# Kernel tuning notes

Hardware: AMD Instinct MI355X
Metric: run time of the kernel (lower is better)

Reference implementation:

```python
import jax, jax.numpy as jnp
import numpy as np

B, C, H, W = 8, 256, 128, 128


def _bilinear_sample(img, gx, gy):
    """F.grid_sample(bilinear, padding_mode='zeros', align_corners=False).
    img: [B,C,H,W]; gx, gy: [B,H,W] normalized coords in [-1,1].
    Returns [B,C,H,W]."""
    Bi, Ci, Hi, Wi = img.shape
    ix = ((gx + 1.0) * Wi - 1.0) * 0.5  # pixel x coord
    iy = ((gy + 1.0) * Hi - 1.0) * 0.5  # pixel y coord
    ix0 = jnp.floor(ix)
    iy0 = jnp.floor(iy)
    wx1 = ix - ix0
    wy1 = iy - iy0
    bidx = jnp.arange(Bi)[:, None, None]

    def gather(iyf, ixf):
        valid = (ixf >= 0) & (ixf < Wi) & (iyf >= 0) & (iyf < Hi)
        iyc = jnp.clip(iyf, 0, Hi - 1).astype(jnp.int32)
        ixc = jnp.clip(ixf, 0, Wi - 1).astype(jnp.int32)
        v = img[bidx, :, iyc, ixc]  # [B,H,W,C]
        return jnp.where(valid[..., None], v, jnp.zeros((), img.dtype))

    v00 = gather(iy0, ix0)
    v01 = gather(iy0, ix0 + 1)
    v10 = gather(iy0 + 1, ix0)
    v11 = gather(iy0 + 1, ix0 + 1)
    w00 = ((1.0 - wy1) * (1.0 - wx1))[..., None]
    w01 = ((1.0 - wy1) * wx1)[..., None]
    w10 = (wy1 * (1.0 - wx1))[..., None]
    w11 = (wy1 * wx1)[..., None]
    out = v00 * w00 + v01 * w01 + v10 * w10 + v11 * w11  # [B,H,W,C]
    return out.transpose(0, 3, 1, 2)


def setup_inputs() -> dict:
    key = jax.random.key(0)
    ks = jax.random.split(key, 7)
    s = 1.0 / np.sqrt(C)
    return {
        "x": jax.random.normal(ks[0], (B, C, H, W), jnp.float32),
        "w_dw": jax.random.normal(ks[1], (C,), jnp.float32) * s,        # depthwise 1x1, no bias
        "w_off": jax.random.normal(ks[2], (2, C), jnp.float32) * s,     # offset 1x1 conv C->2
        "b_off": jax.random.normal(ks[3], (2,), jnp.float32) * 0.1,
        "w_pc": jax.random.normal(ks[4], (C, C), jnp.float32) * s,      # pointwise 1x1, no bias
        "w_W": jax.random.normal(ks[5], (C, C), jnp.float32) * s,       # residual-merge 1x1 conv
        "b_W": jax.random.normal(ks[6], (C,), jnp.float32) * 0.1,
    }


def reference(x, w_dw, w_off, b_off, w_pc, w_W, b_W):
    # offset = tanh(Conv1x1(x)) -> one shared (dx, dy) field (group == inplanes)
    offset = jnp.tanh(jnp.einsum('oc,bchw->bohw', w_off, x) + b_off[None, :, None, None])
    # depthwise 1x1 conv (bias=False) == per-channel scale
    dw = x * w_dw[None, :, None, None]
    # base normalized grid: X varies along W, Y along H (np.meshgrid convention)
    gx_base = jnp.linspace(-1.0, 1.0, W)[None, None, :]  # [1,1,W]
    gy_base = jnp.linspace(-1.0, 1.0, H)[None, :, None]  # [1,H,1]
    gx = jnp.clip(gx_base + offset[:, 0], -1.0, 1.0)  # [B,H,W]
    gy = jnp.clip(gy_base + offset[:, 1], -1.0, 1.0)
    sampled = _bilinear_sample(dw, gx, gy)             # [B,C,H,W]
    out = jnp.einsum('oc,bchw->bohw', w_pc, sampled)   # pointwise conv
    out = jnp.einsum('oc,bchw->bohw', w_W, out) + b_W[None, :, None, None]
    return out + x
```

## Files before the change

### kernel.cpp

```cpp
#include <hip/hip_runtime.h>
#include <hip/hip_bf16.h>

#define Bn 8
#define Cn 256
#define Hn 128
#define Wn 128
#define HWn (Hn * Wn)

typedef __attribute__((ext_vector_type(8))) short bfrag8;
typedef __attribute__((ext_vector_type(8))) unsigned short u16x8;
typedef __attribute__((ext_vector_type(4))) float f32x4;
typedef __attribute__((ext_vector_type(4))) unsigned int u32x4;

__device__ __forceinline__ float bf2f(unsigned short u) {
    unsigned int v = ((unsigned int)u) << 16;
    return __builtin_bit_cast(float, v);
}
__device__ __forceinline__ unsigned short f2bf(float f) {
    unsigned int u = __builtin_bit_cast(unsigned int, f);
    unsigned int lsb = (u >> 16) & 1u;
    u += 0x7fffu + lsb;
    return (unsigned short)(u >> 16);
}

__device__ __forceinline__ void load_lds16(const void* g, void* l) {
    __builtin_amdgcn_global_load_lds(
        (const __attribute__((address_space(1))) unsigned int*)g,
        (__attribute__((address_space(3))) unsigned int*)l,
        16, 0, 0);
}

__global__ __launch_bounds__(256)
void build_wcomb(const float* __restrict__ w_dw,
                 const float* __restrict__ w_pc,
                 const float* __restrict__ w_W,
                 unsigned short* __restrict__ wfrag) {
    const int o = blockIdx.x;
    const int c = threadIdx.x;
    float acc = 0.f;
#pragma unroll 8
    for (int k = 0; k < Cn; ++k)
        acc = fmaf(w_W[o * Cn + k], w_pc[k * Cn + c], acc);
    const int ob = o >> 4, lr = o & 15;
    const int ks = c >> 5, lg = (c & 31) >> 3, e = c & 7;
    const int lane = (lg << 4) + lr;
    wfrag[((((ob << 3) + ks) << 6) + lane) * 8 + e] = f2bf(acc * w_dw[c]);
}

__global__ __launch_bounds__(512, 2)
void prep_kernel(const float* __restrict__ x,
                 const float* __restrict__ w_off,
                 const float* __restrict__ b_off,
                 unsigned short* __restrict__ x_t,
                 float2* __restrict__ coords) {
    __shared__ __align__(16) char tile[256 * 256];
    __shared__ float woT[2][256];
    const int t = threadIdx.x;
    const int lane = t & 63;
    const int wv = t >> 6;
    int blk = blockIdx.x;
    blk = ((blk & 7) << 8) | (blk >> 3);
    const int b = blk >> 8;
    const int p0 = (blk & 255) << 6;
    const float* xp = x + ((size_t)b * Cn) * HWn + p0;

    {
        const int s = t >> 8, c = t & 255;
        woT[s][((c & 7) << 5) | (c >> 3)] = w_off[(s << 8) + c];
    }

    {
        const int r = lane >> 4;
        const int q = lane & 15;
#pragma unroll
        for (int i = 0; i < 8; ++i) {
            const int cbase = (wv << 5) + (i << 2);
            const int c = cbase + r;
            const int swz = (c ^ (c >> 4)) & 15;
            const float* src = xp + (size_t)c * HWn + ((q ^ swz) << 2);
            load_lds16(src, tile + (cbase << 8));
        }
    }
    __syncthreads();

    {
        const int m = lane >> 5;
        const int octet = lane & 31;
#pragma unroll
        for (int i = 0; i < 4; ++i) {
            const int px = (wv << 3) + (i << 1) + m;
            float s0 = 0.f, s1 = 0.f;
            u16x8 res;
#pragma unroll
            for (int j = 0; j < 8; ++j) {
                const int c = (octet << 3) + j;
                const int swz = (c ^ (c >> 4)) & 15;
                const int byte = (c << 8) + ((((px >> 2) ^ swz)) << 4) + ((px & 3) << 2);
                float v = *reinterpret_cast<const float*>(tile + byte);
                s0 = fmaf(v, woT[0][(j << 5) + octet], s0);
                s1 = fmaf(v, woT[1][(j << 5) + octet], s1);
                res[j] = f2bf(v);
            }
            *reinterpret_cast<u16x8*>(
                x_t + ((size_t)(b * HWn + p0 + px)) * Cn + (octet << 3)) = res;

            s0 += __shfl_xor(s0, 1); s0 += __shfl_xor(s0, 2); s0 += __shfl_xor(s0, 4);
            s0 += __shfl_xor(s0, 8); s0 += __shfl_xor(s0, 16);
            s1 += __shfl_xor(s1, 1); s1 += __shfl_xor(s1, 2); s1 += __shfl_xor(s1, 4);
            s1 += __shfl_xor(s1, 8); s1 += __shfl_xor(s1, 16);
            if (octet == 0) {
                float o0 = tanhf(s0 + b_off[0]);
                float o1 = tanhf(s1 + b_off[1]);
                int p = p0 + px;
                int yy = p >> 7, xx = p & 127;
                float gx = fminf(fmaxf(-1.f + xx * (2.f / 127.f) + o0, -1.f), 1.f);
                float gy = fminf(fmaxf(-1.f + yy * (2.f / 127.f) + o1, -1.f), 1.f);
                coords[(size_t)b * HWn + p] = make_float2(gx * 64.f + 63.5f, gy * 64.f + 63.5f);
            }
        }
    }
}

__global__ __launch_bounds__(512, 2)
void main_kernel(const float* __restrict__ x,
                 const float* __restrict__ b_W,
                 const unsigned short* __restrict__ x_t,
                 const float2* __restrict__ coords,
                 const unsigned short* __restrict__ wfrag,
                 float* __restrict__ out) {
    __shared__ __align__(16) char As[4][32 * 512];
    __shared__ __align__(16) float4 wts[32];
    const int t = threadIdx.x;
    const int lane = t & 63;
    const int wid = t >> 6;
    int blk = blockIdx.x;
    blk = ((blk & 7) << 9) | (blk >> 3);
    const int b = blk >> 9;
    const int p0 = (blk & 511) << 5;
    const size_t pixbase = (size_t)b * HWn + p0;
    const unsigned short* xtb = x_t + (size_t)b * HWn * Cn;

    if (t < 32) {
        float2 co = coords[pixbase + t];
        float ix = co.x, iy = co.y;
        float fx = floorf(ix), fy = floorf(iy);
        int ix0 = (int)fx, iy0 = (int)fy;
        float wx1 = ix - fx, wy1 = iy - fy;
        float wx0 = 1.f - wx1, wy0 = 1.f - wy1;
        bool vx0 = (ix0 >= 0) && (ix0 < Wn);
        bool vx1 = (ix0 >= -1) && (ix0 < Wn - 1);
        bool vy0 = (iy0 >= 0) && (iy0 < Hn);
        bool vy1 = (iy0 >= -1) && (iy0 < Hn - 1);
        float4 w;
        w.x = (vy0 && vx0) ? wy0 * wx0 : 0.f;
        w.y = (vy0 && vx1) ? wy0 * wx1 : 0.f;
        w.z = (vy1 && vx0) ? wy1 * wx0 : 0.f;
        w.w = (vy1 && vx1) ? wy1 * wx1 : 0.f;
        wts[t] = w;
    }

    {
        const int hp = lane >> 5;
        const int j = lane & 31;
        float2 co[2];
#pragma unroll
        for (int i = 0; i < 2; ++i)
            co[i] = coords[pixbase + (wid << 2) + (i << 1) + hp];

#pragma unroll
        for (int i = 0; i < 2; ++i) {
            const int p = (wid << 2) + (i << 1);
            const int px = p + hp;
            float ix = co[i].x, iy = co[i].y;
            int ix0 = (int)floorf(ix), iy0 = (int)floorf(iy);
            int cx0 = min(max(ix0, 0), Wn - 1), cx1 = min(max(ix0 + 1, 0), Wn - 1);
            int cy0 = min(max(iy0, 0), Hn - 1), cy1 = min(max(iy0 + 1, 0), Hn - 1);
            const int gch = (j ^ (px & 15)) << 3;
            const unsigned short* s00 = xtb + (size_t)(cy0 * Wn + cx0) * Cn + gch;
            const unsigned short* s01 = xtb + (size_t)(cy0 * Wn + cx1) * Cn + gch;
            const unsigned short* s10 = xtb + (size_t)(cy1 * Wn + cx0) * Cn + gch;
            const unsigned short* s11 = xtb + (size_t)(cy1 * Wn + cx1) * Cn + gch;
            load_lds16(s00, &As[0][p << 9]);
            load_lds16(s01, &As[1][p << 9]);
            load_lds16(s10, &As[2][p << 9]);
            load_lds16(s11, &As[3][p << 9]);
        }
    }
    __syncthreads();

    {
        const int px = t >> 4;
        const float4 w = wts[px];
#pragma unroll
        for (int q = 0; q < 2; ++q) {
            const int kc = (t & 15) + (q << 4);
            const int off = (px << 9) + ((kc ^ (px & 15)) << 4);
            u16x8 c00 = *reinterpret_cast<const u16x8*>(&As[0][off]);
            u16x8 c01 = *reinterpret_cast<const u16x8*>(&As[1][off]);
            u16x8 c10 = *reinterpret_cast<const u16x8*>(&As[2][off]);
            u16x8 c11 = *reinterpret_cast<const u16x8*>(&As[3][off]);
            u16x8 res;
#pragma unroll
            for (int e = 0; e < 8; ++e) {
                float r = w.x * bf2f(c00[e]) + w.y * bf2f(c01[e])
                        + w.z * bf2f(c10[e]) + w.w * bf2f(c11[e]);
                res[e] = f2bf(r);
            }
            *reinterpret_cast<u16x8*>(&As[0][off]) = res;
        }
    }
    __syncthreads();

    const int lr = lane & 15;
    const int lg = lane >> 4;
    f32x4 acc[2][2];
#pragma unroll
    for (int m = 0; m < 2; ++m)
#pragma unroll
        for (int n = 0; n < 2; ++n)
            acc[m][n] = (f32x4){0.f, 0.f, 0.f, 0.f};

#pragma unroll
    for (int ks = 0; ks < 8; ++ks) {
        bfrag8 a[2], bb[2];
        const int kc = (ks << 2) + lg;
#pragma unroll
        for (int n = 0; n < 2; ++n) {
            const int pr = (n << 4) + lr;
            const int off = (pr << 9) + ((kc ^ (pr & 15)) << 4);
            bb[n] = *reinterpret_cast<const bfrag8*>(&As[0][off]);
        }
#pragma unroll
        for (int m = 0; m < 2; ++m) {
            const int ob = (wid << 1) + m;
            const unsigned short* src = wfrag + ((((ob << 3) + ks) << 6) + lane) * 8;
            a[m] = *reinterpret_cast<const bfrag8*>(src);
        }
#pragma unroll
        for (int m = 0; m < 2; ++m)
#pragma unroll
            for (int n = 0; n < 2; ++n)
                acc[m][n] = __builtin_amdgcn_mfma_f32_16x16x32_bf16(a[m], bb[n], acc[m][n], 0, 0, 0);
    }

#pragma unroll
    for (int m = 0; m < 2; ++m) {
#pragma unroll
        for (int r = 0; r < 4; ++r) {
            int o = (wid << 5) + (m << 4) + (lg << 2) + r;
            float bw = b_W[o];
            size_t rowbase = ((size_t)b * Cn + o) * HWn + p0;
#pragma unroll
            for (int n = 0; n < 2; ++n) {
                size_t idx = rowbase + (n << 4) + lr;
                __builtin_nontemporal_store(acc[m][n][r] + bw + x[idx], &out[idx]);
            }
        }
    }
}

extern "C" void kernel_launch(void* const* d_in, const int* in_sizes, int n_in,
                              void* d_out, int out_size, void* d_ws, size_t ws_size,
                              hipStream_t stream) {
    const float* x     = (const float*)d_in[0];
    const float* w_dw  = (const float*)d_in[1];
    const float* w_off = (const float*)d_in[2];
    const float* b_off = (const float*)d_in[3];
    const float* w_pc  = (const float*)d_in[4];
    const float* w_W   = (const float*)d_in[5];
    const float* b_W   = (const float*)d_in[6];
    float* out = (float*)d_out;

    char* ws = (char*)d_ws;
    unsigned short* x_t   = (unsigned short*)ws;
    float2* coords        = (float2*)(ws + 67108864);
    unsigned short* wcomb = (unsigned short*)(ws + 67108864 + 1048576);

    build_wcomb<<<dim3(256), dim3(256), 0, stream>>>(w_dw, w_pc, w_W, wcomb);
    prep_kernel<<<dim3(2048), dim3(512), 0, stream>>>(x, w_off, b_off, x_t, coords);
    main_kernel<<<dim3(4096), dim3(512), 0, stream>>>(x, b_W, x_t, coords, wcomb, out);
}
```

Before: 116.2 us.

## Shrink prep kernel tiles to 32 pixels and stage channels in two passes

The prep transpose kernel now uses 256-thread blocks over 32 pixels and loads channels in two 128-channel passes through a 16KB LDS tile instead of a 64KB one. Offset-conv partial sums are carried across the passes and reduced once at the end. The smaller LDS footprint allows many more resident blocks per CU, which should hide load latency better. In exchange there are more blocks, extra barriers, and narrower 8-byte stores to x_t.

Measured after the change: 114.0 us. Within noise of the previous version (-1.8%).

```diff
diff --git a/kernel.cpp b/kernel.cpp
--- a/kernel.cpp
+++ b/kernel.cpp
@@ -9,6 +9,7 @@
 
 typedef __attribute__((ext_vector_type(8))) short bfrag8;
 typedef __attribute__((ext_vector_type(8))) unsigned short u16x8;
+typedef __attribute__((ext_vector_type(4))) unsigned short u16x4;
 typedef __attribute__((ext_vector_type(4))) float f32x4;
 typedef __attribute__((ext_vector_type(4))) unsigned int u32x4;
 
@@ -47,76 +48,87 @@
     wfrag[((((ob << 3) + ks) << 6) + lane) * 8 + e] = f2bf(acc * w_dw[c]);
 }
 
-__global__ __launch_bounds__(512, 2)
+__global__ __launch_bounds__(256, 8)
 void prep_kernel(const float* __restrict__ x,
                  const float* __restrict__ w_off,
                  const float* __restrict__ b_off,
                  unsigned short* __restrict__ x_t,
                  float2* __restrict__ coords) {
-    __shared__ __align__(16) char tile[256 * 256];
+    __shared__ __align__(16) char tile[128 * 128];
     __shared__ float woT[2][256];
     const int t = threadIdx.x;
     const int lane = t & 63;
     const int wv = t >> 6;
     int blk = blockIdx.x;
-    blk = ((blk & 7) << 8) | (blk >> 3);
-    const int b = blk >> 8;
-    const int p0 = (blk & 255) << 6;
+    blk = ((blk & 7) << 9) | (blk >> 3);
+    const int b = blk >> 9;
+    const int p0 = (blk & 511) << 5;
     const float* xp = x + ((size_t)b * Cn) * HWn + p0;
 
     {
-        const int s = t >> 8, c = t & 255;
-        woT[s][((c & 7) << 5) | (c >> 3)] = w_off[(s << 8) + c];
-    }
-
-    {
-        const int r = lane >> 4;
-        const int q = lane & 15;
-#pragma unroll
-        for (int i = 0; i < 8; ++i) {
-            const int cbase = (wv << 5) + (i << 2);
-            const int c = cbase + r;
-            const int swz = (c ^ (c >> 4)) & 15;
-            const float* src = xp + (size_t)c * HWn + ((q ^ swz) << 2);
-            load_lds16(src, tile + (cbase << 8));
-        }
-    }
-    __syncthreads();
-
-    {
-        const int m = lane >> 5;
-        const int octet = lane & 31;
+        const int pass = t >> 7, cl = t & 127;
+        const int octet = cl >> 2, j = cl & 3;
+#pragma unroll
+        for (int s = 0; s < 2; ++s)
+            woT[s][(pass << 7) + (j << 5) + octet] = w_off[(s << 8) + t];
+    }
+
+    const int m = lane >> 5;
+    const int octet = lane & 31;
+    float s0[4] = {0.f, 0.f, 0.f, 0.f}, s1[4] = {0.f, 0.f, 0.f, 0.f};
+
+#pragma unroll
+    for (int pass = 0; pass < 2; ++pass) {
+        {
+            const int r = lane >> 3;
+            const int q = lane & 7;
+#pragma unroll
+            for (int i = 0; i < 4; ++i) {
+                const int cbase = (wv << 5) + (i << 3);
+                const int c = cbase + r;
+                const int swz = (c ^ (c >> 3)) & 7;
+                const float* src = xp + (size_t)((pass << 7) + c) * HWn + ((q ^ swz) << 2);
+                load_lds16(src, tile + (cbase << 7));
+            }
+        }
+        __syncthreads();
+
 #pragma unroll
         for (int i = 0; i < 4; ++i) {
             const int px = (wv << 3) + (i << 1) + m;
-            float s0 = 0.f, s1 = 0.f;
-            u16x8 res;
-#pragma unroll
-            for (int j = 0; j < 8; ++j) {
-                const int c = (octet << 3) + j;
-                const int swz = (c ^ (c >> 4)) & 15;
-                const int byte = (c << 8) + ((((px >> 2) ^ swz)) << 4) + ((px & 3) << 2);
+            u16x4 res;
+#pragma unroll
+            for (int j = 0; j < 4; ++j) {
+                const int c = (octet << 2) + j;
+                const int swz = (c ^ (c >> 3)) & 7;
+                const int byte = (c << 7) + ((((px >> 2) ^ swz)) << 4) + ((px & 3) << 2);
                 float v = *reinterpret_cast<const float*>(tile + byte);
-                s0 = fmaf(v, woT[0][(j << 5) + octet], s0);
-                s1 = fmaf(v, woT[1][(j << 5) + octet], s1);
+                s0[i] = fmaf(v, woT[0][(pass << 7) + (j << 5) + octet], s0[i]);
+                s1[i] = fmaf(v, woT[1][(pass << 7) + (j << 5) + octet], s1[i]);
                 res[j] = f2bf(v);
             }
-            *reinterpret_cast<u16x8*>(
-                x_t + ((size_t)(b * HWn + p0 + px)) * Cn + (octet << 3)) = res;
-
-            s0 += __shfl_xor(s0, 1); s0 += __shfl_xor(s0, 2); s0 += __shfl_xor(s0, 4);
-            s0 += __shfl_xor(s0, 8); s0 += __shfl_xor(s0, 16);
-            s1 += __shfl_xor(s1, 1); s1 += __shfl_xor(s1, 2); s1 += __shfl_xor(s1, 4);
-            s1 += __shfl_xor(s1, 8); s1 += __shfl_xor(s1, 16);
-            if (octet == 0) {
-                float o0 = tanhf(s0 + b_off[0]);
-                float o1 = tanhf(s1 + b_off[1]);
-                int p = p0 + px;
-                int yy = p >> 7, xx = p & 127;
-                float gx = fminf(fmaxf(-1.f + xx * (2.f / 127.f) + o0, -1.f), 1.f);
-                float gy = fminf(fmaxf(-1.f + yy * (2.f / 127.f) + o1, -1.f), 1.f);
-                coords[(size_t)b * HWn + p] = make_float2(gx * 64.f + 63.5f, gy * 64.f + 63.5f);
-            }
+            *reinterpret_cast<u16x4*>(
+                x_t + ((size_t)(b * HWn + p0 + px)) * Cn + (pass << 7) + (octet << 2)) = res;
+        }
+        __syncthreads();
+    }
+
+#pragma unroll
+    for (int i = 0; i < 4; ++i) {
+        float a = s0[i], c = s1[i];
+        a += __shfl_xor(a, 1); a += __shfl_xor(a, 2); a += __shfl_xor(a, 4);
+        a += __shfl_xor(a, 8); a += __shfl_xor(a, 16);
+        c += __shfl_xor(c, 1); c += __shfl_xor(c, 2); c += __shfl_xor(c, 4);
+        c += __shfl_xor(c, 8); c += __shfl_xor(c, 16);
+        if (octet == 0) {
+            const int px = (wv << 3) + (i << 1) + m;
+            float o0 = tanhf(a + b_off[0]);
+            float o1 = tanhf(c + b_off[1]);
+            int p = p0 + px;
+            int yy = p >> 7, xx = p & 127;
+            float gx = fminf(fmaxf(-1.f + xx * (2.f / 127.f) + o0, -1.f), 1.f);
+            float gy = fminf(fmaxf(-1.f + yy * (2.f / 127.f) + o1, -1.f), 1.f);
+            coords[(size_t)b * HWn + p] = make_float2(gx * 64.f + 63.5f, gy * 64.f + 63.5f);
         }
     }
 }
@@ -277,6 +289,6 @@
     unsigned short* wcomb = (unsigned short*)(ws + 67108864 + 1048576);
 
     build_wcomb<<<dim3(256), dim3(256), 0, stream>>>(w_dw, w_pc, w_W, wcomb);
-    prep_kernel<<<dim3(2048), dim3(512), 0, stream>>>(x, w_off, b_off, x_t, coords);
+    prep_kernel<<<dim3(4096), dim3(256), 0, stream>>>(x, w_off, b_off, x_t, coords);
     main_kernel<<<dim3(4096), dim3(512), 0, stream>>>(x, b_W, x_t, coords, wcomb, out);
 }
```
